# Kernel tuning notes

Hardware: AMD Instinct MI355X
Metric: run time of the kernel (lower is better)

## Reference

```python
import jax, jax.numpy as jnp
import numpy as np


def setup_inputs() -> dict:
    key = jax.random.key(0)
    k1, k2, k3 = jax.random.split(key, 3)
    B, S, H = 32, 2048, 1024
    hidden = jax.random.normal(k1, (B, H), dtype=jnp.float32)
    encoder_outputs = jax.random.normal(k2, (B, S, H), dtype=jnp.float32)
    W_in = jax.random.normal(k3, (H, H), dtype=jnp.float32) * (1.0 / np.sqrt(H))
    return {"hidden": hidden, "encoder_outputs": encoder_outputs, "W_in": W_in}


def reference(hidden, encoder_outputs, W_in):
    # linear_in: nn.Linear(H, H, bias=False) -> hidden @ W_in.T  [B, H]
    h = hidden @ W_in.T
    # scores: bmm(encoder_outputs [B,S,H], h [B,H,1]) -> [B,S]
    scores = jnp.einsum("bsh,bh->bs", encoder_outputs, h)
    attn_w = jax.nn.softmax(scores, axis=-1)  # [B, S]
    # context: bmm(attn_w [B,1,S], encoder_outputs [B,S,H]) -> [B, H]
    context = jnp.einsum("bs,bsh->bh", attn_w, encoder_outputs)
    return (context, attn_w)
```

## Files before the change

### kernel.cpp

```cpp
#include <hip/hip_runtime.h>
#include <math.h>

constexpr int Bb = 32;
constexpr int Ss = 2048;
constexpr int Hh = 1024;
constexpr int SC = 32;
constexpr int CPB = Ss / SC;
constexpr int NBLK = Bb * CPB;

__global__ __launch_bounds__(256) void gemv_h_kernel(const float* __restrict__ hidden,
                                                     const float* __restrict__ W,
                                                     float* __restrict__ h)
{
    int tid  = threadIdx.x;
    int wid  = blockIdx.x * 4 + (tid >> 6);
    int lane = tid & 63;
    int b = wid >> 10;
    int i = wid & (Hh - 1);
    const float4* wr = reinterpret_cast<const float4*>(W + (size_t)i * Hh);
    const float4* hd = reinterpret_cast<const float4*>(hidden + (size_t)b * Hh);
    float d = 0.f;
#pragma unroll
    for (int k = 0; k < 4; ++k) {
        float4 wv = wr[lane + 64 * k];
        float4 hv = hd[lane + 64 * k];
        d += wv.x * hv.x + wv.y * hv.y + wv.z * hv.z + wv.w * hv.w;
    }
#pragma unroll
    for (int off = 32; off > 0; off >>= 1) d += __shfl_xor(d, off, 64);
    if (lane == 0) h[wid] = d;
}

__global__ __launch_bounds__(256) void attn_partial_kernel(const float* __restrict__ enc,
                                                           const float* __restrict__ h,
                                                           float* __restrict__ scores,
                                                           float* __restrict__ pm,
                                                           float* __restrict__ pl,
                                                           float* __restrict__ pctx)
{
    int blk   = blockIdx.x;
    int b     = blk / CPB;
    int chunk = blk % CPB;
    int s0    = chunk * SC;
    int tid   = threadIdx.x;
    int wave  = tid >> 6;
    int lane  = tid & 63;

    float4 hf[4];
    const float4* h4 = reinterpret_cast<const float4*>(h + (size_t)b * Hh);
#pragma unroll
    for (int k = 0; k < 4; ++k) hf[k] = h4[lane + 64 * k];

    float m = -INFINITY;
    float l = 0.f;
    float4 ctx[4];
#pragma unroll
    for (int k = 0; k < 4; ++k) ctx[k] = make_float4(0.f, 0.f, 0.f, 0.f);

    for (int r = 0; r < 8; ++r) {
        int s = s0 + wave * 8 + r;
        const float4* e4 = reinterpret_cast<const float4*>(enc + ((size_t)b * Ss + s) * Hh);
        float4 ev[4];
#pragma unroll
        for (int k = 0; k < 4; ++k) ev[k] = e4[lane + 64 * k];
        float d = 0.f;
#pragma unroll
        for (int k = 0; k < 4; ++k)
            d += ev[k].x * hf[k].x + ev[k].y * hf[k].y + ev[k].z * hf[k].z + ev[k].w * hf[k].w;
#pragma unroll
        for (int off = 32; off > 0; off >>= 1) d += __shfl_xor(d, off, 64);
        if (lane == 0) scores[(size_t)b * Ss + s] = d;

        if (d > m) {
            float c = __expf(m - d);
            l *= c;
#pragma unroll
            for (int k = 0; k < 4; ++k) {
                ctx[k].x *= c; ctx[k].y *= c; ctx[k].z *= c; ctx[k].w *= c;
            }
            m = d;
        }
        float p = __expf(d - m);
        l += p;
#pragma unroll
        for (int k = 0; k < 4; ++k) {
            ctx[k].x += p * ev[k].x; ctx[k].y += p * ev[k].y;
            ctx[k].z += p * ev[k].z; ctx[k].w += p * ev[k].w;
        }
    }

    __shared__ float lds_ctx[4][Hh];
    __shared__ float lds_m[4], lds_l[4];
    float4* ldsrow = reinterpret_cast<float4*>(lds_ctx[wave]);
#pragma unroll
    for (int k = 0; k < 4; ++k) ldsrow[64 * k + lane] = ctx[k];
    if (lane == 0) { lds_m[wave] = m; lds_l[wave] = l; }
    __syncthreads();

    float M = fmaxf(fmaxf(lds_m[0], lds_m[1]), fmaxf(lds_m[2], lds_m[3]));
    float L = 0.f;
    float4 acc = make_float4(0.f, 0.f, 0.f, 0.f);
#pragma unroll
    for (int w = 0; w < 4; ++w) {
        float c = __expf(lds_m[w] - M);
        L += c * lds_l[w];
        float4 v = reinterpret_cast<float4*>(lds_ctx[w])[tid];
        acc.x += c * v.x; acc.y += c * v.y; acc.z += c * v.z; acc.w += c * v.w;
    }
    reinterpret_cast<float4*>(pctx + (size_t)blk * Hh)[tid] = acc;
    if (tid == 0) { pm[blk] = M; pl[blk] = L; }
}

__global__ __launch_bounds__(256) void combine_kernel(const float* __restrict__ pm,
                                                      const float* __restrict__ pl,
                                                      const float* __restrict__ pctx,
                                                      float* __restrict__ out_ctx,
                                                      float* __restrict__ Mb,
                                                      float* __restrict__ Lb)
{
    int b   = blockIdx.x;
    int tid = threadIdx.x;
    const float* mrow = pm + (size_t)b * CPB;
    const float* lrow = pl + (size_t)b * CPB;

    float M = -INFINITY;
    for (int c = 0; c < CPB; ++c) M = fmaxf(M, mrow[c]);
    float L = 0.f;
    float4 acc = make_float4(0.f, 0.f, 0.f, 0.f);
    for (int c = 0; c < CPB; ++c) {
        float sc = __expf(mrow[c] - M);
        L += sc * lrow[c];
        float4 v = reinterpret_cast<const float4*>(pctx + ((size_t)b * CPB + c) * Hh)[tid];
        acc.x += sc * v.x; acc.y += sc * v.y; acc.z += sc * v.z; acc.w += sc * v.w;
    }
    float inv = 1.f / L;
    float4 o = make_float4(acc.x * inv, acc.y * inv, acc.z * inv, acc.w * inv);
    reinterpret_cast<float4*>(out_ctx + (size_t)b * Hh)[tid] = o;
    if (tid == 0) { Mb[b] = M; Lb[b] = L; }
}

__global__ __launch_bounds__(256) void finish_attn_kernel(const float* __restrict__ scores,
                                                          const float* __restrict__ Mb,
                                                          const float* __restrict__ Lb,
                                                          float* __restrict__ attn_out)
{
    int idx = blockIdx.x * 256 + threadIdx.x;
    int b = idx >> 11;
    float inv = 1.f / Lb[b];
    attn_out[idx] = __expf(scores[idx] - Mb[b]) * inv;
}

extern "C" void kernel_launch(void* const* d_in, const int* in_sizes, int n_in,
                              void* d_out, int out_size, void* d_ws, size_t ws_size,
                              hipStream_t stream) {
    const float* hidden = (const float*)d_in[0];
    const float* enc    = (const float*)d_in[1];
    const float* W_in   = (const float*)d_in[2];

    float* out_ctx  = (float*)d_out;
    float* out_attn = (float*)d_out + Bb * Hh;

    float* ws     = (float*)d_ws;
    float* h      = ws;
    float* scores = ws + 32768;
    float* pm     = ws + 98304;
    float* pl     = ws + 100352;
    float* pctx   = ws + 102400;
    float* Mb     = ws + 102400 + (size_t)NBLK * Hh;
    float* Lb     = Mb + Bb;
    (void)in_sizes; (void)n_in; (void)out_size; (void)ws_size;

    gemv_h_kernel<<<(Bb * Hh) / 4, 256, 0, stream>>>(hidden, W_in, h);
    attn_partial_kernel<<<NBLK, 256, 0, stream>>>(enc, h, scores, pm, pl, pctx);
    combine_kernel<<<Bb, 256, 0, stream>>>(pm, pl, pctx, out_ctx, Mb, Lb);
    finish_attn_kernel<<<(Bb * Ss) / 256, 256, 0, stream>>>(scores, Mb, Lb, out_attn);
}
```

Before: 67.05 us.

## Double sequence chunk size, reorder GEMV waves, and widen combine parallelism

Raises the per-block sequence chunk from 32 to 64 rows, which halves the number of partial-context blocks and the partial buffer written and re-read by the combine step. The GEMV is remapped so each block's four waves share one W row across four batches, improving cache reuse of W. The combine kernel now uses four blocks per batch, each handling 256 columns with scalar loads, instead of one block per batch. The trade-off is fewer attention blocks (1024) and longer serial loops per wave.

```diff
diff --git a/kernel.cpp b/kernel.cpp
--- a/kernel.cpp
+++ b/kernel.cpp
@@ -4,7 +4,7 @@
 constexpr int Bb = 32;
 constexpr int Ss = 2048;
 constexpr int Hh = 1024;
-constexpr int SC = 32;
+constexpr int SC = 64;
 constexpr int CPB = Ss / SC;
 constexpr int NBLK = Bb * CPB;
 
@@ -13,10 +13,11 @@
                                                      float* __restrict__ h)
 {
     int tid  = threadIdx.x;
-    int wid  = blockIdx.x * 4 + (tid >> 6);
+    int wave = tid >> 6;
     int lane = tid & 63;
-    int b = wid >> 10;
-    int i = wid & (Hh - 1);
+    int i  = blockIdx.x >> 3;
+    int bg = blockIdx.x & 7;
+    int b  = bg * 4 + wave;
     const float4* wr = reinterpret_cast<const float4*>(W + (size_t)i * Hh);
     const float4* hd = reinterpret_cast<const float4*>(hidden + (size_t)b * Hh);
     float d = 0.f;
@@ -28,7 +29,7 @@
     }
 #pragma unroll
     for (int off = 32; off > 0; off >>= 1) d += __shfl_xor(d, off, 64);
-    if (lane == 0) h[wid] = d;
+    if (lane == 0) h[(size_t)b * Hh + i] = d;
 }
 
 __global__ __launch_bounds__(256) void attn_partial_kernel(const float* __restrict__ enc,
@@ -57,8 +58,8 @@
 #pragma unroll
     for (int k = 0; k < 4; ++k) ctx[k] = make_float4(0.f, 0.f, 0.f, 0.f);
 
-    for (int r = 0; r < 8; ++r) {
-        int s = s0 + wave * 8 + r;
+    for (int r = 0; r < 16; ++r) {
+        int s = s0 + wave * 16 + r;
         const float4* e4 = reinterpret_cast<const float4*>(enc + ((size_t)b * Ss + s) * Hh);
         float4 ev[4];
 #pragma unroll
@@ -118,25 +119,30 @@
                                                       float* __restrict__ Mb,
                                                       float* __restrict__ Lb)
 {
-    int b   = blockIdx.x;
+    int b   = blockIdx.x >> 2;
+    int j   = blockIdx.x & 3;
     int tid = threadIdx.x;
+    int col = j * 256 + tid;
+
     const float* mrow = pm + (size_t)b * CPB;
     const float* lrow = pl + (size_t)b * CPB;
 
     float M = -INFINITY;
+#pragma unroll
     for (int c = 0; c < CPB; ++c) M = fmaxf(M, mrow[c]);
+    float e[CPB];
     float L = 0.f;
-    float4 acc = make_float4(0.f, 0.f, 0.f, 0.f);
+#pragma unroll
     for (int c = 0; c < CPB; ++c) {
-        float sc = __expf(mrow[c] - M);
-        L += sc * lrow[c];
-        float4 v = reinterpret_cast<const float4*>(pctx + ((size_t)b * CPB + c) * Hh)[tid];
-        acc.x += sc * v.x; acc.y += sc * v.y; acc.z += sc * v.z; acc.w += sc * v.w;
+        e[c] = __expf(mrow[c] - M);
+        L += e[c] * lrow[c];
     }
-    float inv = 1.f / L;
-    float4 o = make_float4(acc.x * inv, acc.y * inv, acc.z * inv, acc.w * inv);
-    reinterpret_cast<float4*>(out_ctx + (size_t)b * Hh)[tid] = o;
-    if (tid == 0) { Mb[b] = M; Lb[b] = L; }
+    float acc = 0.f;
+#pragma unroll 4
+    for (int c = 0; c < CPB; ++c)
+        acc += e[c] * pctx[((size_t)b * CPB + c) * Hh + col];
+    out_ctx[(size_t)b * Hh + col] = acc / L;
+    if (j == 0 && tid == 0) { Mb[b] = M; Lb[b] = L; }
 }
 
 __global__ __launch_bounds__(256) void finish_attn_kernel(const float* __restrict__ scores,
@@ -164,14 +170,14 @@
     float* h      = ws;
     float* scores = ws + 32768;
     float* pm     = ws + 98304;
-    float* pl     = ws + 100352;
-    float* pctx   = ws + 102400;
-    float* Mb     = ws + 102400 + (size_t)NBLK * Hh;
+    float* pl     = ws + 99328;
+    float* pctx   = ws + 100352;
+    float* Mb     = pctx + (size_t)NBLK * Hh;
     float* Lb     = Mb + Bb;
     (void)in_sizes; (void)n_in; (void)out_size; (void)ws_size;
 
-    gemv_h_kernel<<<(Bb * Hh) / 4, 256, 0, stream>>>(hidden, W_in, h);
+    gemv_h_kernel<<<Hh * (Bb / 4), 256, 0, stream>>>(hidden, W_in, h);
     attn_partial_kernel<<<NBLK, 256, 0, stream>>>(enc, h, scores, pm, pl, pctx);
-    combine_kernel<<<Bb, 256, 0, stream>>>(pm, pl, pctx, out_ctx, Mb, Lb);
+    combine_kernel<<<Bb * (Hh / 256), 256, 0, stream>>>(pm, pl, pctx, out_ctx, Mb, Lb);
     finish_attn_kernel<<<(Bb * Ss) / 256, 256, 0, stream>>>(scores, Mb, Lb, out_attn);
 }
```

Result: slower. 68.55 us (+2.2%).
